# Performance work log

Hardware: AMD Instinct MI355X
Metric: run time of the kernel (lower is better)

Reference implementation:

```python
import jax, jax.numpy as jnp
import numpy as np

Q_N = 65536   # queries
KV_N = 65536  # keys/values
C = 256       # channels
H = 8         # heads
D = C // H
N_E = 524288  # edges
SCALE = 1.0 / np.sqrt(C).astype(np.float32)  # sim_scale/sqrt(num_ch), sim_scale=1
LN_EPS = 1e-5


def setup_inputs() -> dict:
    key = jax.random.key(0)
    ks = jax.random.split(key, 8)
    q = jax.random.normal(ks[0], (Q_N, C), jnp.float32)
    k = jax.random.normal(ks[1], (KV_N, C), jnp.float32)
    bias = jax.random.normal(ks[2], (N_E, H), jnp.float32) * 0.1
    src = jax.random.randint(ks[3], (N_E,), 0, KV_N)
    dst = jnp.sort(jax.random.randint(ks[4], (N_E,), 0, Q_N))
    wq = jax.random.normal(ks[5], (C, C), jnp.float32) * 0.02
    wk = jax.random.normal(ks[6], (C, C), jnp.float32) * 0.02
    wo = jax.random.normal(ks[7], (C, C), jnp.float32) * 0.02
    return {
        "q": q, "k": k, "bias": bias,
        "ln_w": jnp.ones((C,), jnp.float32), "ln_b": jnp.zeros((C,), jnp.float32),
        "wq": wq, "bq": jnp.zeros((C,), jnp.float32),
        "wk": wk, "bk": jnp.zeros((C,), jnp.float32),
        "wo": wo, "bo": jnp.zeros((C,), jnp.float32),
        "src": src, "dst": dst,
    }


def _layernorm(x, w, b):
    mu = jnp.mean(x, axis=-1, keepdims=True)
    var = jnp.var(x, axis=-1, keepdims=True)
    return (x - mu) * jax.lax.rsqrt(var + LN_EPS) * w + b


def reference(q, k, bias, ln_w, ln_b, wq, bq, wk, bk, wo, bo, src, dst):
    residual = q
    qn = _layernorm(q, ln_w, ln_b)           # norm_loc='pre'
    qp = qn @ wq.T + bq                       # [Q, C]
    kp = k @ wk.T + bk                        # [KV, C]; same_kv -> v = kp
    # gather per-edge, split heads: [N, H, D]
    qe = qp[dst].reshape(N_E, H, D)
    ke = kp[src].reshape(N_E, H, D)
    sim = (jnp.sum(qe * ke, axis=-1) + bias) * SCALE   # [N, H]
    # segment-max per dst (init -inf, matching index_reduce amax)
    max_sim = jax.ops.segment_max(sim, dst, num_segments=Q_N)  # [Q, H]
    e = jnp.exp(sim - max_sim[dst])
    wsum = 1e-8 + jax.ops.segment_sum(e, dst, num_segments=Q_N)  # [Q, H]
    weights = e / wsum[dst]                   # [N, H]
    out_e = (ke * weights[..., None]).reshape(N_E, C)  # weighted values (v=k)
    out = jax.ops.segment_sum(out_e, dst, num_segments=Q_N)  # [Q, C]
    out = out @ wo.T + bo + residual
    return out, weights
```

## Files before the change

kernel.cpp:

```cpp
#include <hip/hip_runtime.h>
#include <cmath>

#define QN    65536
#define KVN   65536
#define CD    256
#define NH    8
#define NE    524288
#define SCL   0.0625f
#define LNEPS 1e-5f
#define LOG2E 1.4426950408889634f

typedef __bf16 bf16x8 __attribute__((ext_vector_type(8)));
typedef float  f32x4  __attribute__((ext_vector_type(4)));

__device__ __forceinline__ float b2f(ushort u) {
    return __builtin_bit_cast(float, (unsigned)u << 16);
}
__device__ __forceinline__ ushort f2bf(float f) {
    unsigned u = __builtin_bit_cast(unsigned, f);
    return (ushort)((u + 0x7FFFu + ((u >> 16) & 1u)) >> 16);
}

#if __has_builtin(__builtin_amdgcn_exp2f)
__device__ __forceinline__ float fexp2(float x) { return __builtin_amdgcn_exp2f(x); }
#else
__device__ __forceinline__ float fexp2(float x) {
    float r; asm volatile("v_exp_f32 %0, %1" : "=v"(r) : "v"(x)); return r;
}
#endif

#define GLD16(g, l) __builtin_amdgcn_global_load_lds( \
    (const __attribute__((address_space(1))) unsigned int*)(const void*)(g), \
    (__attribute__((address_space(3))) unsigned int*)(void*)(l), 16, 0, 0)

#define LNB   (QN / 4)
#define RLB   (NE / 256)
__global__ __launch_bounds__(256) void prep_k(const float* __restrict__ q,
                                              const float* __restrict__ lnw,
                                              const float* __restrict__ lnb,
                                              const float* __restrict__ wq,
                                              const float* __restrict__ wk,
                                              const float* __restrict__ wo,
                                              const int* __restrict__ dst,
                                              ushort* __restrict__ qn,
                                              ushort* __restrict__ wb,
                                              int* __restrict__ row_lo) {
    const int blk = blockIdx.x;
    if (blk < LNB) {
        int row  = (blk << 2) + (threadIdx.x >> 6);
        int lane = threadIdx.x & 63;
        float4 v = *(const float4*)(q + (size_t)row * CD + (lane << 2));
        float s  = v.x + v.y + v.z + v.w;
        float s2 = v.x * v.x + v.y * v.y + v.z * v.z + v.w * v.w;
        #pragma unroll
        for (int m = 1; m < 64; m <<= 1) {
            s  += __shfl_xor(s, m);
            s2 += __shfl_xor(s2, m);
        }
        float mu   = s * (1.0f / CD);
        float rstd = rsqrtf(s2 * (1.0f / CD) - mu * mu + LNEPS);
        float4 w = *(const float4*)(lnw + (lane << 2));
        float4 b = *(const float4*)(lnb + (lane << 2));
        ushort4 o;
        o.x = f2bf((v.x - mu) * rstd * w.x + b.x);
        o.y = f2bf((v.y - mu) * rstd * w.y + b.y);
        o.z = f2bf((v.z - mu) * rstd * w.z + b.z);
        o.w = f2bf((v.w - mu) * rstd * w.w + b.w);
        *(ushort4*)(qn + (size_t)row * CD + (lane << 2)) = o;
    } else if (blk < LNB + 192) {
        int idx4 = ((blk - LNB) * 256 + threadIdx.x) * 4;
        int mat  = idx4 >> 16;
        int off  = idx4 & 65535;
        const float* src = (mat == 0) ? wq : (mat == 1) ? wk : wo;
        float4 v = *(const float4*)(src + off);
        ushort4 o;
        o.x = f2bf(v.x); o.y = f2bf(v.y); o.z = f2bf(v.z); o.w = f2bf(v.w);
        *(ushort4*)(wb + idx4) = o;
    } else {
        int e = (blk - LNB - 192) * 256 + threadIdx.x;
        int d     = dst[e];
        int dprev = (e == 0) ? -1 : dst[e - 1];
        for (int qq = dprev + 1; qq <= d; ++qq) row_lo[qq] = e;
        if (e == NE - 1)
            for (int qq = d + 1; qq <= QN; ++qq) row_lo[qq] = NE;
    }
}

template<int EPI>
__global__ __launch_bounds__(256) void gemm_bf16_k(const ushort* __restrict__ A0,
                                                   const float* __restrict__ Afp,
                                                   const ushort* __restrict__ B0,
                                                   const ushort* __restrict__ B1,
                                                   const float* __restrict__ bias0,
                                                   const float* __restrict__ bias1,
                                                   const float* __restrict__ resid,
                                                   void* __restrict__ C0,
                                                   void* __restrict__ C1) {
    const bool conv = (blockIdx.z != 0);
    const ushort* B    = conv ? B1 : B0;
    const float*  bias = conv ? bias1 : bias0;
    void*         Cout = conv ? C1 : C0;

    __shared__ __align__(16) ushort As[2][128 * 32];
    __shared__ __align__(16) ushort Bs[2][128 * 32];
    const int t    = threadIdx.x;
    const int lane = t & 63;
    const int wid  = t >> 6;
    const int wm   = wid & 1, wn = wid >> 1;
    const size_t bm = (size_t)blockIdx.x * 128;
    const size_t bn = (size_t)blockIdx.y * 128;

    const int sr = t >> 2;
    const int sc = (t & 3) * 8;

    f32x4 acc[4][4] = {};

    {
        const ushort* gb = B + (bn + sr) * CD + sc;
        GLD16(gb,           &Bs[0][wid * 512]);
        GLD16(gb + 64 * CD, &Bs[0][2048 + wid * 512]);
        if (conv) {
            const float* ga = Afp + (bm + sr) * CD + sc;
            float4 a0 = *(const float4*)(ga);
            float4 a1 = *(const float4*)(ga + 4);
            float4 a2 = *(const float4*)(ga + 64 * CD);
            float4 a3 = *(const float4*)(ga + 64 * CD + 4);
            union { ushort u[8]; uint4 v; } p0, p1;
            p0.u[0] = f2bf(a0.x); p0.u[1] = f2bf(a0.y); p0.u[2] = f2bf(a0.z); p0.u[3] = f2bf(a0.w);
            p0.u[4] = f2bf(a1.x); p0.u[5] = f2bf(a1.y); p0.u[6] = f2bf(a1.z); p0.u[7] = f2bf(a1.w);
            p1.u[0] = f2bf(a2.x); p1.u[1] = f2bf(a2.y); p1.u[2] = f2bf(a2.z); p1.u[3] = f2bf(a2.w);
            p1.u[4] = f2bf(a3.x); p1.u[5] = f2bf(a3.y); p1.u[6] = f2bf(a3.z); p1.u[7] = f2bf(a3.w);
            *(uint4*)&As[0][sr * 32 + sc]        = p0.v;
            *(uint4*)&As[0][(sr + 64) * 32 + sc] = p1.v;
        } else {
            const ushort* ga = A0 + (bm + sr) * CD + sc;
            GLD16(ga,           &As[0][wid * 512]);
            GLD16(ga + 64 * CD, &As[0][2048 + wid * 512]);
        }
    }
    __syncthreads();

    for (int kt = 0; kt < 8; ++kt) {
        const int cur = kt & 1;
        float4 a0n, a1n, a2n, a3n;
        if (kt < 7) {
            const int kb = (kt + 1) * 32;
            const ushort* gb = B + (bn + sr) * CD + kb + sc;
            GLD16(gb,           &Bs[cur ^ 1][wid * 512]);
            GLD16(gb + 64 * CD, &Bs[cur ^ 1][2048 + wid * 512]);
            if (conv) {
                const float* ga = Afp + (bm + sr) * CD + kb + sc;
                a0n = *(const float4*)(ga);
                a1n = *(const float4*)(ga + 4);
                a2n = *(const float4*)(ga + 64 * CD);
                a3n = *(const float4*)(ga + 64 * CD + 4);
            } else {
                const ushort* ga = A0 + (bm + sr) * CD + kb + sc;
                GLD16(ga,           &As[cur ^ 1][wid * 512]);
                GLD16(ga + 64 * CD, &As[cur ^ 1][2048 + wid * 512]);
            }
        }
        const int kq = (lane >> 4) * 8;
        bf16x8 af[4], bg[4];
        #pragma unroll
        for (int mi = 0; mi < 4; ++mi)
            af[mi] = *(const bf16x8*)&As[cur][(wm * 64 + mi * 16 + (lane & 15)) * 32 + kq];
        #pragma unroll
        for (int ni = 0; ni < 4; ++ni)
            bg[ni] = *(const bf16x8*)&Bs[cur][(wn * 64 + ni * 16 + (lane & 15)) * 32 + kq];
        #pragma unroll
        for (int mi = 0; mi < 4; ++mi)
            #pragma unroll
            for (int ni = 0; ni < 4; ++ni)
                acc[mi][ni] = __builtin_amdgcn_mfma_f32_16x16x32_bf16(af[mi], bg[ni], acc[mi][ni], 0, 0, 0);
        if (kt < 7 && conv) {
            union { ushort u[8]; uint4 v; } p0, p1;
            p0.u[0] = f2bf(a0n.x); p0.u[1] = f2bf(a0n.y); p0.u[2] = f2bf(a0n.z); p0.u[3] = f2bf(a0n.w);
            p0.u[4] = f2bf(a1n.x); p0.u[5] = f2bf(a1n.y); p0.u[6] = f2bf(a1n.z); p0.u[7] = f2bf(a1n.w);
            p1.u[0] = f2bf(a2n.x); p1.u[1] = f2bf(a2n.y); p1.u[2] = f2bf(a2n.z); p1.u[3] = f2bf(a2n.w);
            p1.u[4] = f2bf(a3n.x); p1.u[5] = f2bf(a3n.y); p1.u[6] = f2bf(a3n.z); p1.u[7] = f2bf(a3n.w);
            *(uint4*)&As[cur ^ 1][sr * 32 + sc]        = p0.v;
            *(uint4*)&As[cur ^ 1][(sr + 64) * 32 + sc] = p1.v;
        }
        __syncthreads();
    }

    const int col0 = lane & 15;
    #pragma unroll
    for (int ni = 0; ni < 4; ++ni) {
        const size_t col = bn + wn * 64 + ni * 16 + col0;
        const float bv = bias[col];
        #pragma unroll
        for (int mi = 0; mi < 4; ++mi) {
            #pragma unroll
            for (int r = 0; r < 4; ++r) {
                const size_t row = bm + wm * 64 + mi * 16 + (lane >> 4) * 4 + r;
                float v = acc[mi][ni][r] + bv;
                if (EPI == 0) {
                    ((ushort*)Cout)[row * CD + col] = f2bf(v);
                } else {
                    ((float*)Cout)[row * CD + col] = v + resid[row * CD + col];
                }
            }
        }
    }
}

__global__ __launch_bounds__(64) void edge_attn_k(const ushort* __restrict__ qp,
                                                  const ushort* __restrict__ kp,
                                                  const float* __restrict__ bias,
                                                  const int* __restrict__ src,
                                                  const int* __restrict__ row_lo,
                                                  ushort* __restrict__ ao,
                                                  float* __restrict__ simw) {
    const int q    = blockIdx.x;
    const int lane = threadIdx.x;
    const int lo = row_lo[q];
    const int hi = row_lo[q + 1];
    const int deg = hi - lo;
    const float SC2 = SCL * LOG2E;

    ushort4 qu = *(const ushort4*)(qp + (size_t)q * CD + (lane << 2));
    float4 qv = {b2f(qu.x) * SC2, b2f(qu.y) * SC2, b2f(qu.z) * SC2, b2f(qu.w) * SC2};
    float4 acc = {0.f, 0.f, 0.f, 0.f};
    float m = -INFINITY, s = 0.f;
    float wval0 = 0.f, wval1 = 0.f;

    for (int base = lo; base < hi; base += 8) {
        const int cnum = (base - lo) >> 3;
        int sv = 0;
        if (lane < 8 && base + lane < hi) sv = src[base + lane];
        float bch = 0.f;
        if (lane < (hi - base) * 8) bch = bias[(size_t)base * NH + lane] * SC2;
        ushort4 ku[8];
        #pragma unroll
        for (int i = 0; i < 8; ++i) {
            if (base + i < hi) {
                int sidx = __shfl(sv, i);
                ku[i] = *(const ushort4*)(kp + (size_t)sidx * CD + (lane << 2));
            }
        }
        #pragma unroll
        for (int i = 0; i < 8; ++i) {
            if (base + i < hi) {
                float4 kv = {b2f(ku[i].x), b2f(ku[i].y), b2f(ku[i].z), b2f(ku[i].w)};
                float d = qv.x * kv.x + qv.y * kv.y + qv.z * kv.z + qv.w * kv.w;
                d += __shfl_xor(d, 1);
                d += __shfl_xor(d, 2);
                d += __shfl_xor(d, 4);
                float bvi = __shfl(bch, (i << 3) + (lane >> 3));
                float sim = d + bvi;
                float tw = __shfl(sim, (lane & 7) << 3);
                bool mine = ((lane >> 3) == i);
                if (deg <= 16) {
                    if (cnum == 0) wval0 = mine ? tw : wval0;
                    else           wval1 = mine ? tw : wval1;
                } else {
                    wval0 = mine ? tw : wval0;
                }
                float mnew  = fmaxf(m, sim);
                float scale = fexp2(m - mnew);
                float ex    = fexp2(sim - mnew);
                s = s * scale + ex;
                acc.x = acc.x * scale + ex * kv.x;
                acc.y = acc.y * scale + ex * kv.y;
                acc.z = acc.z * scale + ex * kv.z;
                acc.w = acc.w * scale + ex * kv.w;
                m = mnew;
            }
        }
        if (deg > 16) {
            int lim = hi - base; if (lim > 8) lim = 8;
            if (lane < lim * 8) simw[(size_t)base * NH + lane] = wval0;
        }
    }

    float ws  = s + 1e-8f;
    float inv = 1.0f / ws;
    ushort4 o;
    o.x = f2bf(acc.x * inv);
    o.y = f2bf(acc.y * inv);
    o.z = f2bf(acc.z * inv);
    o.w = f2bf(acc.w * inv);
    *(ushort4*)(ao + (size_t)q * CD + (lane << 2)) = o;

    if (deg > 0) {
        const float mm = __shfl(m,   (lane & 7) << 3);
        const float ii = __shfl(inv, (lane & 7) << 3);
        if (deg <= 8) {
            if (lane < deg * 8)
                simw[(size_t)lo * NH + lane] = fexp2(wval0 - mm) * ii;
        } else if (deg <= 16) {
            simw[(size_t)lo * NH + lane] = fexp2(wval0 - mm) * ii;
            if (lane < (deg - 8) * 8)
                simw[(size_t)(lo + 8) * NH + lane] = fexp2(wval1 - mm) * ii;
        } else {
            asm volatile("s_waitcnt vmcnt(0)" ::: "memory");
            for (int i = lane; i < deg * 8; i += 64) {
                size_t idx = (size_t)lo * NH + i;
                float v = simw[idx];
                simw[idx] = fexp2(v - mm) * ii;
            }
        }
    }
}

extern "C" void kernel_launch(void* const* d_in, const int* in_sizes, int n_in,
                              void* d_out, int out_size, void* d_ws, size_t ws_size,
                              hipStream_t stream) {
    const float* q    = (const float*)d_in[0];
    const float* k    = (const float*)d_in[1];
    const float* bias = (const float*)d_in[2];
    const float* lnw  = (const float*)d_in[3];
    const float* lnb  = (const float*)d_in[4];
    const float* wq   = (const float*)d_in[5];
    const float* bq   = (const float*)d_in[6];
    const float* wk   = (const float*)d_in[7];
    const float* bk   = (const float*)d_in[8];
    const float* wo   = (const float*)d_in[9];
    const float* bo   = (const float*)d_in[10];
    const int*   src  = (const int*)d_in[11];
    const int*   dst  = (const int*)d_in[12];

    float* out_m = (float*)d_out;
    float* out_w = out_m + (size_t)QN * CD;

    ushort* qn_b = (ushort*)d_ws;
    ushort* qp_b = qn_b + (size_t)QN * CD;
    ushort* kp_b = qp_b + (size_t)QN * CD;
    ushort* wb   = kp_b + (size_t)KVN * CD;
    int*    rowlo = (int*)(wb + 3 * 65536);

    prep_k<<<dim3(LNB + 192 + RLB), dim3(256), 0, stream>>>(
        q, lnw, lnb, wq, wk, wo, dst, qn_b, wb, rowlo);

    gemm_bf16_k<0><<<dim3(QN / 128, 2, 2), dim3(256), 0, stream>>>(
        qn_b, k, wb, wb + 65536, bq, bk, nullptr, qp_b, kp_b);

    edge_attn_k<<<dim3(QN), dim3(64), 0, stream>>>(
        qp_b, kp_b, bias, src, rowlo, qn_b , out_w);

    gemm_bf16_k<1><<<dim3(QN / 128, 2, 1), dim3(256), 0, stream>>>(
        qn_b, nullptr, wb + 131072, wb + 131072, bo, bo, q, out_m, out_m);
}
```

Baseline: 181.7 us.

## Deepen GEMM shared-memory pipeline to four stages with explicit vmcnt waits

Replaces the double-buffered K loop in the bf16 GEMM with a 4-slot ring that prefetches three K-tiles ahead, using a fully unrolled macro and hand-written s_waitcnt vmcnt/s_barrier sequences tuned per iteration. The aim is to hide global-to-LDS load latency better than the single-tile lookahead did. In exchange it doubles LDS use (64KB per block), which may cut occupancy, and relies on hand-counted vmcnt values that must match the emitted load instructions exactly.

```diff
diff --git a/kernel.cpp b/kernel.cpp
--- a/kernel.cpp
+++ b/kernel.cpp
@@ -101,8 +101,8 @@
     const float*  bias = conv ? bias1 : bias0;
     void*         Cout = conv ? C1 : C0;
 
-    __shared__ __align__(16) ushort As[2][128 * 32];
-    __shared__ __align__(16) ushort Bs[2][128 * 32];
+    __shared__ __align__(16) ushort As[4][128 * 32];
+    __shared__ __align__(16) ushort Bs[4][128 * 32];
     const int t    = threadIdx.x;
     const int lane = t & 63;
     const int wid  = t >> 6;
@@ -115,75 +115,101 @@
 
     f32x4 acc[4][4] = {};
 
-    {
-        const ushort* gb = B + (bn + sr) * CD + sc;
-        GLD16(gb,           &Bs[0][wid * 512]);
-        GLD16(gb + 64 * CD, &Bs[0][2048 + wid * 512]);
-        if (conv) {
-            const float* ga = Afp + (bm + sr) * CD + sc;
-            float4 a0 = *(const float4*)(ga);
-            float4 a1 = *(const float4*)(ga + 4);
-            float4 a2 = *(const float4*)(ga + 64 * CD);
-            float4 a3 = *(const float4*)(ga + 64 * CD + 4);
-            union { ushort u[8]; uint4 v; } p0, p1;
-            p0.u[0] = f2bf(a0.x); p0.u[1] = f2bf(a0.y); p0.u[2] = f2bf(a0.z); p0.u[3] = f2bf(a0.w);
-            p0.u[4] = f2bf(a1.x); p0.u[5] = f2bf(a1.y); p0.u[6] = f2bf(a1.z); p0.u[7] = f2bf(a1.w);
-            p1.u[0] = f2bf(a2.x); p1.u[1] = f2bf(a2.y); p1.u[2] = f2bf(a2.z); p1.u[3] = f2bf(a2.w);
-            p1.u[4] = f2bf(a3.x); p1.u[5] = f2bf(a3.y); p1.u[6] = f2bf(a3.z); p1.u[7] = f2bf(a3.w);
-            *(uint4*)&As[0][sr * 32 + sc]        = p0.v;
-            *(uint4*)&As[0][(sr + 64) * 32 + sc] = p1.v;
-        } else {
-            const ushort* ga = A0 + (bm + sr) * CD + sc;
-            GLD16(ga,           &As[0][wid * 512]);
-            GLD16(ga + 64 * CD, &As[0][2048 + wid * 512]);
-        }
-    }
-    __syncthreads();
-
-    for (int kt = 0; kt < 8; ++kt) {
-        const int cur = kt & 1;
-        float4 a0n, a1n, a2n, a3n;
-        if (kt < 7) {
-            const int kb = (kt + 1) * 32;
-            const ushort* gb = B + (bn + sr) * CD + kb + sc;
-            GLD16(gb,           &Bs[cur ^ 1][wid * 512]);
-            GLD16(gb + 64 * CD, &Bs[cur ^ 1][2048 + wid * 512]);
-            if (conv) {
-                const float* ga = Afp + (bm + sr) * CD + kb + sc;
-                a0n = *(const float4*)(ga);
-                a1n = *(const float4*)(ga + 4);
-                a2n = *(const float4*)(ga + 64 * CD);
-                a3n = *(const float4*)(ga + 64 * CD + 4);
-            } else {
-                const ushort* ga = A0 + (bm + sr) * CD + kb + sc;
-                GLD16(ga,           &As[cur ^ 1][wid * 512]);
-                GLD16(ga + 64 * CD, &As[cur ^ 1][2048 + wid * 512]);
-            }
-        }
-        const int kq = (lane >> 4) * 8;
-        bf16x8 af[4], bg[4];
-        #pragma unroll
-        for (int mi = 0; mi < 4; ++mi)
-            af[mi] = *(const bf16x8*)&As[cur][(wm * 64 + mi * 16 + (lane & 15)) * 32 + kq];
-        #pragma unroll
-        for (int ni = 0; ni < 4; ++ni)
-            bg[ni] = *(const bf16x8*)&Bs[cur][(wn * 64 + ni * 16 + (lane & 15)) * 32 + kq];
-        #pragma unroll
-        for (int mi = 0; mi < 4; ++mi)
-            #pragma unroll
-            for (int ni = 0; ni < 4; ++ni)
-                acc[mi][ni] = __builtin_amdgcn_mfma_f32_16x16x32_bf16(af[mi], bg[ni], acc[mi][ni], 0, 0, 0);
-        if (kt < 7 && conv) {
-            union { ushort u[8]; uint4 v; } p0, p1;
-            p0.u[0] = f2bf(a0n.x); p0.u[1] = f2bf(a0n.y); p0.u[2] = f2bf(a0n.z); p0.u[3] = f2bf(a0n.w);
-            p0.u[4] = f2bf(a1n.x); p0.u[5] = f2bf(a1n.y); p0.u[6] = f2bf(a1n.z); p0.u[7] = f2bf(a1n.w);
-            p1.u[0] = f2bf(a2n.x); p1.u[1] = f2bf(a2n.y); p1.u[2] = f2bf(a2n.z); p1.u[3] = f2bf(a2n.w);
-            p1.u[4] = f2bf(a3n.x); p1.u[5] = f2bf(a3n.y); p1.u[6] = f2bf(a3n.z); p1.u[7] = f2bf(a3n.w);
-            *(uint4*)&As[cur ^ 1][sr * 32 + sc]        = p0.v;
-            *(uint4*)&As[cur ^ 1][(sr + 64) * 32 + sc] = p1.v;
-        }
-        __syncthreads();
-    }
+    if (conv) {
+        const float* ga = Afp + (bm + sr) * CD + sc;
+        float4 a0 = *(const float4*)(ga);
+        float4 a1 = *(const float4*)(ga + 4);
+        float4 a2 = *(const float4*)(ga + 64 * CD);
+        float4 a3 = *(const float4*)(ga + 64 * CD + 4);
+        #pragma unroll
+        for (int s = 0; s < 3; ++s) {
+            const ushort* gb = B + (bn + sr) * CD + s * 32 + sc;
+            GLD16(gb,           &Bs[s][wid * 512]);
+            GLD16(gb + 64 * CD, &Bs[s][2048 + wid * 512]);
+        }
+        union { ushort u[8]; uint4 v; } p0, p1;
+        p0.u[0] = f2bf(a0.x); p0.u[1] = f2bf(a0.y); p0.u[2] = f2bf(a0.z); p0.u[3] = f2bf(a0.w);
+        p0.u[4] = f2bf(a1.x); p0.u[5] = f2bf(a1.y); p0.u[6] = f2bf(a1.z); p0.u[7] = f2bf(a1.w);
+        p1.u[0] = f2bf(a2.x); p1.u[1] = f2bf(a2.y); p1.u[2] = f2bf(a2.z); p1.u[3] = f2bf(a2.w);
+        p1.u[4] = f2bf(a3.x); p1.u[5] = f2bf(a3.y); p1.u[6] = f2bf(a3.z); p1.u[7] = f2bf(a3.w);
+        *(uint4*)&As[0][sr * 32 + sc]        = p0.v;
+        *(uint4*)&As[0][(sr + 64) * 32 + sc] = p1.v;
+    } else {
+        #pragma unroll
+        for (int s = 0; s < 3; ++s) {
+            const ushort* gb = B  + (bn + sr) * CD + s * 32 + sc;
+            const ushort* ga = A0 + (bm + sr) * CD + s * 32 + sc;
+            GLD16(gb,           &Bs[s][wid * 512]);
+            GLD16(gb + 64 * CD, &Bs[s][2048 + wid * 512]);
+            GLD16(ga,           &As[s][wid * 512]);
+            GLD16(ga + 64 * CD, &As[s][2048 + wid * 512]);
+        }
+    }
+
+#define ITER(KT, VMZ0, VMZ1)                                                          \
+  {                                                                                   \
+    float4 a0n, a1n, a2n, a3n;                                                        \
+    if (conv) {                                                                       \
+      if ((KT) < 7) {                                                                 \
+        const float* ga = Afp + (bm + sr) * CD + ((KT) + 1) * 32 + sc;                \
+        a0n = *(const float4*)(ga);                                                   \
+        a1n = *(const float4*)(ga + 4);                                               \
+        a2n = *(const float4*)(ga + 64 * CD);                                         \
+        a3n = *(const float4*)(ga + 64 * CD + 4);                                     \
+      }                                                                               \
+      if ((KT) + 3 <= 7) {                                                            \
+        const ushort* gb = B + (bn + sr) * CD + ((KT) + 3) * 32 + sc;                 \
+        GLD16(gb,           &Bs[((KT) + 3) & 3][wid * 512]);                          \
+        GLD16(gb + 64 * CD, &Bs[((KT) + 3) & 3][2048 + wid * 512]);                   \
+      }                                                                               \
+      asm volatile("s_waitcnt vmcnt(" #VMZ1 ") lgkmcnt(0)\ns_barrier" ::: "memory");  \
+    } else {                                                                          \
+      if ((KT) + 3 <= 7) {                                                            \
+        const ushort* gb = B  + (bn + sr) * CD + ((KT) + 3) * 32 + sc;                \
+        const ushort* ga = A0 + (bm + sr) * CD + ((KT) + 3) * 32 + sc;                \
+        GLD16(gb,           &Bs[((KT) + 3) & 3][wid * 512]);                          \
+        GLD16(gb + 64 * CD, &Bs[((KT) + 3) & 3][2048 + wid * 512]);                   \
+        GLD16(ga,           &As[((KT) + 3) & 3][wid * 512]);                          \
+        GLD16(ga + 64 * CD, &As[((KT) + 3) & 3][2048 + wid * 512]);                   \
+      }                                                                               \
+      asm volatile("s_waitcnt vmcnt(" #VMZ0 ") lgkmcnt(0)\ns_barrier" ::: "memory");  \
+    }                                                                                 \
+    {                                                                                 \
+      const int kq = (lane >> 4) * 8;                                                 \
+      bf16x8 af[4], bg[4];                                                            \
+      _Pragma("unroll")                                                               \
+      for (int mi = 0; mi < 4; ++mi)                                                  \
+        af[mi] = *(const bf16x8*)&As[(KT) & 3][(wm * 64 + mi * 16 + (lane & 15)) * 32 + kq]; \
+      _Pragma("unroll")                                                               \
+      for (int ni = 0; ni < 4; ++ni)                                                  \
+        bg[ni] = *(const bf16x8*)&Bs[(KT) & 3][(wn * 64 + ni * 16 + (lane & 15)) * 32 + kq]; \
+      _Pragma("unroll")                                                               \
+      for (int mi = 0; mi < 4; ++mi)                                                  \
+        _Pragma("unroll")                                                             \
+        for (int ni = 0; ni < 4; ++ni)                                                \
+          acc[mi][ni] = __builtin_amdgcn_mfma_f32_16x16x32_bf16(af[mi], bg[ni], acc[mi][ni], 0, 0, 0); \
+    }                                                                                 \
+    if (conv && (KT) < 7) {             \
+      union { ushort u[8]; uint4 v; } p0, p1;                                         \
+      p0.u[0] = f2bf(a0n.x); p0.u[1] = f2bf(a0n.y); p0.u[2] = f2bf(a0n.z); p0.u[3] = f2bf(a0n.w); \
+      p0.u[4] = f2bf(a1n.x); p0.u[5] = f2bf(a1n.y); p0.u[6] = f2bf(a1n.z); p0.u[7] = f2bf(a1n.w); \
+      p1.u[0] = f2bf(a2n.x); p1.u[1] = f2bf(a2n.y); p1.u[2] = f2bf(a2n.z); p1.u[3] = f2bf(a2n.w); \
+      p1.u[4] = f2bf(a3n.x); p1.u[5] = f2bf(a3n.y); p1.u[6] = f2bf(a3n.z); p1.u[7] = f2bf(a3n.w); \
+      *(uint4*)&As[((KT) + 1) & 3][sr * 32 + sc]        = p0.v;                       \
+      *(uint4*)&As[((KT) + 1) & 3][(sr + 64) * 32 + sc] = p1.v;                       \
+    }                                                                                 \
+    asm volatile("s_waitcnt lgkmcnt(0)\ns_barrier" ::: "memory");                     \
+  }
+
+    ITER(0, 12, 10)
+    ITER(1, 12, 10)
+    ITER(2, 12, 10)
+    ITER(3, 12, 10)
+    ITER(4, 12, 10)
+    ITER(5,  8,  8)
+    ITER(6,  4,  6)
+    ITER(7,  0,  0)
+#undef ITER
 
     const int col0 = lane & 15;
     #pragma unroll
```

New measurement: 178.3 us. No clear change (-1.9%).

## Rewrite projection GEMMs as persistent multi-tile kernels with resident B and deep A prefetch

Applied to the files above, without the earlier changes.

The GEMMs are replaced by a 512-thread kernel in which each block keeps the full 128-column weight slice in LDS. It streams several 128-row A tiles through an 8-stage ring with explicit vmcnt waits and barriers, so loads for the next tile overlap the current tile's MFMAs. The K input is converted to bf16 in the prep kernel, using the output buffer as scratch, instead of being converted inside the GEMM. The epilogue now uses vectorized bias and residual accesses. In exchange the code depends on hand-counted waitcnt values, uses more LDS per block and runs fewer, longer blocks.

```diff
diff --git a/kernel.cpp b/kernel.cpp
--- a/kernel.cpp
+++ b/kernel.cpp
@@ -36,6 +36,7 @@
 #define LNB   (QN / 4)
 #define RLB   (NE / 256)
 __global__ __launch_bounds__(256) void prep_k(const float* __restrict__ q,
+                                              const float* __restrict__ k,
                                               const float* __restrict__ lnw,
                                               const float* __restrict__ lnb,
                                               const float* __restrict__ wq,
@@ -43,6 +44,7 @@
                                               const float* __restrict__ wo,
                                               const int* __restrict__ dst,
                                               ushort* __restrict__ qn,
+                                              ushort* __restrict__ kb,
                                               ushort* __restrict__ wb,
                                               int* __restrict__ row_lo) {
     const int blk = blockIdx.x;
@@ -76,134 +78,142 @@
         ushort4 o;
         o.x = f2bf(v.x); o.y = f2bf(v.y); o.z = f2bf(v.z); o.w = f2bf(v.w);
         *(ushort4*)(wb + idx4) = o;
-    } else {
+    } else if (blk < LNB + 192 + RLB) {
         int e = (blk - LNB - 192) * 256 + threadIdx.x;
         int d     = dst[e];
         int dprev = (e == 0) ? -1 : dst[e - 1];
         for (int qq = dprev + 1; qq <= d; ++qq) row_lo[qq] = e;
         if (e == NE - 1)
             for (int qq = d + 1; qq <= QN; ++qq) row_lo[qq] = NE;
+    } else {
+        int row  = ((blk - LNB - 192 - RLB) << 2) + (threadIdx.x >> 6);
+        int lane = threadIdx.x & 63;
+        float4 v = *(const float4*)(k + (size_t)row * CD + (lane << 2));
+        ushort4 o;
+        o.x = f2bf(v.x); o.y = f2bf(v.y); o.z = f2bf(v.z); o.w = f2bf(v.w);
+        *(ushort4*)(kb + (size_t)row * CD + (lane << 2)) = o;
     }
 }
 
-template<int EPI>
-__global__ __launch_bounds__(256) void gemm_bf16_k(const ushort* __restrict__ A0,
-                                                   const float* __restrict__ Afp,
-                                                   const ushort* __restrict__ B0,
-                                                   const ushort* __restrict__ B1,
-                                                   const float* __restrict__ bias0,
-                                                   const float* __restrict__ bias1,
-                                                   const float* __restrict__ resid,
-                                                   void* __restrict__ C0,
-                                                   void* __restrict__ C1) {
-    const bool conv = (blockIdx.z != 0);
-    const ushort* B    = conv ? B1 : B0;
-    const float*  bias = conv ? bias1 : bias0;
-    void*         Cout = conv ? C1 : C0;
-
-    __shared__ __align__(16) ushort As[2][128 * 32];
-    __shared__ __align__(16) ushort Bs[2][128 * 32];
+template<int EPI, int NT>
+__global__ __launch_bounds__(512) void gemm2_k(const ushort* __restrict__ A0,
+                                               const ushort* __restrict__ A1,
+                                               const ushort* __restrict__ B0,
+                                               const ushort* __restrict__ B1,
+                                               const float* __restrict__ bias0,
+                                               const float* __restrict__ bias1,
+                                               const float* __restrict__ resid,
+                                               void* __restrict__ C0,
+                                               void* __restrict__ C1) {
+    const bool second = (blockIdx.z != 0);
+    const ushort* Ap   = second ? A1 : A0;
+    const ushort* B    = second ? B1 : B0;
+    const float*  bias = second ? bias1 : bias0;
+    void*         Cout = second ? C1 : C0;
+
+    __shared__ __align__(16) ushort Bs[8][4096];
+    __shared__ __align__(16) ushort As[8][4096];
+
     const int t    = threadIdx.x;
     const int lane = t & 63;
     const int wid  = t >> 6;
-    const int wm   = wid & 1, wn = wid >> 1;
-    const size_t bm = (size_t)blockIdx.x * 128;
-    const size_t bn = (size_t)blockIdx.y * 128;
+    const int wm   = wid & 1;
+    const int wn   = wid >> 1;
+    const size_t bn  = (size_t)blockIdx.y * 128;
+    size_t bm = (size_t)blockIdx.x * (NT * 128);
 
     const int sr = t >> 2;
     const int sc = (t & 3) * 8;
 
-    f32x4 acc[4][4] = {};
-
-    {
-        const ushort* gb = B + (bn + sr) * CD + sc;
-        GLD16(gb,           &Bs[0][wid * 512]);
-        GLD16(gb + 64 * CD, &Bs[0][2048 + wid * 512]);
-        if (conv) {
-            const float* ga = Afp + (bm + sr) * CD + sc;
-            float4 a0 = *(const float4*)(ga);
-            float4 a1 = *(const float4*)(ga + 4);
-            float4 a2 = *(const float4*)(ga + 64 * CD);
-            float4 a3 = *(const float4*)(ga + 64 * CD + 4);
-            union { ushort u[8]; uint4 v; } p0, p1;
-            p0.u[0] = f2bf(a0.x); p0.u[1] = f2bf(a0.y); p0.u[2] = f2bf(a0.z); p0.u[3] = f2bf(a0.w);
-            p0.u[4] = f2bf(a1.x); p0.u[5] = f2bf(a1.y); p0.u[6] = f2bf(a1.z); p0.u[7] = f2bf(a1.w);
-            p1.u[0] = f2bf(a2.x); p1.u[1] = f2bf(a2.y); p1.u[2] = f2bf(a2.z); p1.u[3] = f2bf(a2.w);
-            p1.u[4] = f2bf(a3.x); p1.u[5] = f2bf(a3.y); p1.u[6] = f2bf(a3.z); p1.u[7] = f2bf(a3.w);
-            *(uint4*)&As[0][sr * 32 + sc]        = p0.v;
-            *(uint4*)&As[0][(sr + 64) * 32 + sc] = p1.v;
-        } else {
-            const ushort* ga = A0 + (bm + sr) * CD + sc;
-            GLD16(ga,           &As[0][wid * 512]);
-            GLD16(ga + 64 * CD, &As[0][2048 + wid * 512]);
-        }
+    constexpr int E = (EPI == 0) ? 8 : 16;
+
+    f32x4 acc[4][2] = {};
+    f32x4 biasv[2];
+    #pragma unroll
+    for (int ni = 0; ni < 2; ++ni)
+        biasv[ni] = *(const f32x4*)(bias + bn + wn * 32 + ni * 16 + ((lane >> 4) << 2));
+
+    #pragma unroll
+    for (int s = 0; s < 8; ++s)
+        GLD16(B + (bn + sr) * CD + (s << 5) + sc, &Bs[s][wid << 9]);
+    #pragma unroll
+    for (int s = 0; s < 6; ++s)
+        GLD16(Ap + (bm + sr) * CD + (s << 5) + sc, &As[s][wid << 9]);
+    asm volatile("" : "+v"(biasv[0]), "+v"(biasv[1]));
+
+#define KSTEP(KT, VM, GUARD)                                                          \
+  {                                                                                   \
+    if (GUARD) {                                                                      \
+      const ushort* ga_ = Ap + (bm + (((KT) >= 2) ? 128 : 0) + sr) * CD               \
+                          + ((((KT) + 6) & 7) << 5) + sc;                             \
+      GLD16(ga_, &As[((KT) + 6) & 7][wid << 9]);                                      \
+    }                                                                                 \
+    asm volatile("s_waitcnt vmcnt(%0) lgkmcnt(0)\n\ts_barrier" :: "i"(VM) : "memory");\
+    {                                                                                 \
+      const int kq_ = (lane >> 4) << 3;                                               \
+      bf16x8 af_[4], bg_[2];                                                          \
+      _Pragma("unroll")                                                               \
+      for (int mi = 0; mi < 4; ++mi)                                                  \
+        af_[mi] = *(const bf16x8*)&As[(KT) & 7][((wm * 64 + mi * 16 + (lane & 15)) << 5) + kq_]; \
+      _Pragma("unroll")                                                               \
+      for (int ni = 0; ni < 2; ++ni)                                                  \
+        bg_[ni] = *(const bf16x8*)&Bs[(KT)][((wn * 32 + ni * 16 + (lane & 15)) << 5) + kq_];     \
+      _Pragma("unroll")                                                               \
+      for (int mi = 0; mi < 4; ++mi)                                                  \
+        _Pragma("unroll")                                                             \
+        for (int ni = 0; ni < 2; ++ni)                                                \
+          acc[mi][ni] = __builtin_amdgcn_mfma_f32_16x16x32_bf16(bg_[ni], af_[mi], acc[mi][ni], 0, 0, 0); \
+    }                                                                                 \
+  }
+
+#define EPILOG()                                                                      \
+  {                                                                                   \
+    _Pragma("unroll")                                                                 \
+    for (int mi = 0; mi < 4; ++mi) {                                                  \
+      const size_t row_ = bm + wm * 64 + mi * 16 + (lane & 15);                       \
+      _Pragma("unroll")                                                               \
+      for (int ni = 0; ni < 2; ++ni) {                                                \
+        const size_t col_ = bn + wn * 32 + ni * 16 + ((lane >> 4) << 2);              \
+        if (EPI == 0) {                                                               \
+          ushort4 o_;                                                                 \
+          o_.x = f2bf(acc[mi][ni][0] + biasv[ni][0]);                                 \
+          o_.y = f2bf(acc[mi][ni][1] + biasv[ni][1]);                                 \
+          o_.z = f2bf(acc[mi][ni][2] + biasv[ni][2]);                                 \
+          o_.w = f2bf(acc[mi][ni][3] + biasv[ni][3]);                                 \
+          *(ushort4*)((ushort*)Cout + row_ * CD + col_) = o_;                         \
+        } else {                                                                      \
+          f32x4 rs_ = *(const f32x4*)(resid + row_ * CD + col_);                      \
+          f32x4 o_;                                                                   \
+          o_[0] = acc[mi][ni][0] + biasv[ni][0] + rs_[0];                             \
+          o_[1] = acc[mi][ni][1] + biasv[ni][1] + rs_[1];                             \
+          o_[2] = acc[mi][ni][2] + biasv[ni][2] + rs_[2];                             \
+          o_[3] = acc[mi][ni][3] + biasv[ni][3] + rs_[3];                             \
+          *(f32x4*)((float*)Cout + row_ * CD + col_) = o_;                            \
+        }                                                                             \
+        acc[mi][ni] = (f32x4){0.f, 0.f, 0.f, 0.f};                                    \
+      }                                                                               \
+    }                                                                                 \
+    asm volatile("" ::: "memory");          \
+  }
+
+    KSTEP(0, 6, 1) KSTEP(1, 6, 1) KSTEP(2, 6, 1) KSTEP(3, 6, 1)
+    KSTEP(4, 6, 1) KSTEP(5, 6, 1) KSTEP(6, 6, 1) KSTEP(7, 6, 1)
+    EPILOG();
+    bm += 128;
+
+    for (int tt = 1; tt < NT - 1; ++tt) {
+        KSTEP(0, 6 + E, 1) KSTEP(1, 6 + E, 1) KSTEP(2, 6 + E, 1) KSTEP(3, 6 + E, 1)
+        KSTEP(4, 6 + E, 1) KSTEP(5, 6 + E, 1) KSTEP(6, 6, 1)     KSTEP(7, 6, 1)
+        EPILOG();
+        bm += 128;
     }
-    __syncthreads();
-
-    for (int kt = 0; kt < 8; ++kt) {
-        const int cur = kt & 1;
-        float4 a0n, a1n, a2n, a3n;
-        if (kt < 7) {
-            const int kb = (kt + 1) * 32;
-            const ushort* gb = B + (bn + sr) * CD + kb + sc;
-            GLD16(gb,           &Bs[cur ^ 1][wid * 512]);
-            GLD16(gb + 64 * CD, &Bs[cur ^ 1][2048 + wid * 512]);
-            if (conv) {
-                const float* ga = Afp + (bm + sr) * CD + kb + sc;
-                a0n = *(const float4*)(ga);
-                a1n = *(const float4*)(ga + 4);
-                a2n = *(const float4*)(ga + 64 * CD);
-                a3n = *(const float4*)(ga + 64 * CD + 4);
-            } else {
-                const ushort* ga = A0 + (bm + sr) * CD + kb + sc;
-                GLD16(ga,           &As[cur ^ 1][wid * 512]);
-                GLD16(ga + 64 * CD, &As[cur ^ 1][2048 + wid * 512]);
-            }
-        }
-        const int kq = (lane >> 4) * 8;
-        bf16x8 af[4], bg[4];
-        #pragma unroll
-        for (int mi = 0; mi < 4; ++mi)
-            af[mi] = *(const bf16x8*)&As[cur][(wm * 64 + mi * 16 + (lane & 15)) * 32 + kq];
-        #pragma unroll
-        for (int ni = 0; ni < 4; ++ni)
-            bg[ni] = *(const bf16x8*)&Bs[cur][(wn * 64 + ni * 16 + (lane & 15)) * 32 + kq];
-        #pragma unroll
-        for (int mi = 0; mi < 4; ++mi)
-            #pragma unroll
-            for (int ni = 0; ni < 4; ++ni)
-                acc[mi][ni] = __builtin_amdgcn_mfma_f32_16x16x32_bf16(af[mi], bg[ni], acc[mi][ni], 0, 0, 0);
-        if (kt < 7 && conv) {
-            union { ushort u[8]; uint4 v; } p0, p1;
-            p0.u[0] = f2bf(a0n.x); p0.u[1] = f2bf(a0n.y); p0.u[2] = f2bf(a0n.z); p0.u[3] = f2bf(a0n.w);
-            p0.u[4] = f2bf(a1n.x); p0.u[5] = f2bf(a1n.y); p0.u[6] = f2bf(a1n.z); p0.u[7] = f2bf(a1n.w);
-            p1.u[0] = f2bf(a2n.x); p1.u[1] = f2bf(a2n.y); p1.u[2] = f2bf(a2n.z); p1.u[3] = f2bf(a2n.w);
-            p1.u[4] = f2bf(a3n.x); p1.u[5] = f2bf(a3n.y); p1.u[6] = f2bf(a3n.z); p1.u[7] = f2bf(a3n.w);
-            *(uint4*)&As[cur ^ 1][sr * 32 + sc]        = p0.v;
-            *(uint4*)&As[cur ^ 1][(sr + 64) * 32 + sc] = p1.v;
-        }
-        __syncthreads();
-    }
-
-    const int col0 = lane & 15;
-    #pragma unroll
-    for (int ni = 0; ni < 4; ++ni) {
-        const size_t col = bn + wn * 64 + ni * 16 + col0;
-        const float bv = bias[col];
-        #pragma unroll
-        for (int mi = 0; mi < 4; ++mi) {
-            #pragma unroll
-            for (int r = 0; r < 4; ++r) {
-                const size_t row = bm + wm * 64 + mi * 16 + (lane >> 4) * 4 + r;
-                float v = acc[mi][ni][r] + bv;
-                if (EPI == 0) {
-                    ((ushort*)Cout)[row * CD + col] = f2bf(v);
-                } else {
-                    ((float*)Cout)[row * CD + col] = v + resid[row * CD + col];
-                }
-            }
-        }
-    }
+
+    KSTEP(0, 6 + E, 1) KSTEP(1, 6 + E, 1) KSTEP(2, 5 + E, 0) KSTEP(3, 4 + E, 0)
+    KSTEP(4, 3 + E, 0) KSTEP(5, 2 + E, 0) KSTEP(6, 1, 0)     KSTEP(7, 0, 0)
+    EPILOG();
+
+#undef KSTEP
+#undef EPILOG
 }
 
 __global__ __launch_bounds__(64) void edge_attn_k(const ushort* __restrict__ qp,
@@ -331,15 +341,17 @@
     ushort* wb   = kp_b + (size_t)KVN * CD;
     int*    rowlo = (int*)(wb + 3 * 65536);
 
-    prep_k<<<dim3(LNB + 192 + RLB), dim3(256), 0, stream>>>(
-        q, lnw, lnb, wq, wk, wo, dst, qn_b, wb, rowlo);
-
-    gemm_bf16_k<0><<<dim3(QN / 128, 2, 2), dim3(256), 0, stream>>>(
-        qn_b, k, wb, wb + 65536, bq, bk, nullptr, qp_b, kp_b);
+    ushort* kb = (ushort*)d_out;
+
+    prep_k<<<dim3(LNB + 192 + RLB + LNB), dim3(256), 0, stream>>>(
+        q, k, lnw, lnb, wq, wk, wo, dst, qn_b, kb, wb, rowlo);
+
+    gemm2_k<0, 8><<<dim3(64, 2, 2), dim3(512), 0, stream>>>(
+        qn_b, kb, wb, wb + 65536, bq, bk, nullptr, qp_b, kp_b);
 
     edge_attn_k<<<dim3(QN), dim3(64), 0, stream>>>(
         qp_b, kp_b, bias, src, rowlo, qn_b , out_w);
 
-    gemm_bf16_k<1><<<dim3(QN / 128, 2, 1), dim3(256), 0, stream>>>(
-        qn_b, nullptr, wb + 131072, wb + 131072, bo, bo, q, out_m, out_m);
-}
+    gemm2_k<1, 4><<<dim3(128, 2, 1), dim3(512), 0, stream>>>(
+        qn_b, qn_b, wb + 131072, wb + 131072, bo, bo, q, out_m, out_m);
+}
```

Result: faster. 170.1 us (-6.4%).
